# Optimization experiments

Measured on AMD Instinct MI355X. Metric: run time of the kernel, lower is better.

The kernel has to match this reference:

```python
import jax, jax.numpy as jnp
import numpy as np

N_NODES = 100000


def gcn_conv(x, W, b, src, dst, num_nodes):
    """PyG GCNConv: self-loops + symmetric norm + linear + scatter-add."""
    loop = jnp.arange(num_nodes, dtype=src.dtype)
    s = jnp.concatenate([src, loop])  # [E+N]
    d = jnp.concatenate([dst, loop])  # [E+N]
    # degree on destination column (edge_weight = 1)
    deg = jax.ops.segment_sum(jnp.ones_like(d, dtype=x.dtype), d,
                              num_segments=num_nodes)
    dinv = jnp.where(deg > 0, jax.lax.rsqrt(deg), 0.0)
    norm = dinv[s] * dinv[d]  # [E+N]
    h = x @ W  # [N, out] project before aggregation
    msg = h[s] * norm[:, None]  # gather + normalize
    out = jax.ops.segment_sum(msg, d, num_segments=num_nodes)  # scatter-add
    return out + b


def setup_inputs() -> dict:
    key = jax.random.key(0)
    k_x, k_e, k_w1, k_b1, k_w2, k_b2 = jax.random.split(key, 6)
    in_channels, hidden, out_dim = 128, 64, 2
    n_edges = 3200000
    x = jax.random.normal(k_x, (N_NODES, in_channels), dtype=jnp.float32)
    edge_index = jax.random.randint(k_e, (2, n_edges), 0, N_NODES, dtype=jnp.int64)
    # Glorot-style init for linear weights, zero bias (PyG default)
    W1 = jax.random.normal(k_w1, (in_channels, hidden), dtype=jnp.float32) * (1.0 / np.sqrt(in_channels))
    b1 = jnp.zeros((hidden,), dtype=jnp.float32)
    W2 = jax.random.normal(k_w2, (hidden, out_dim), dtype=jnp.float32) * (1.0 / np.sqrt(hidden))
    b2 = jnp.zeros((out_dim,), dtype=jnp.float32)
    return {"x": x, "edge_index": edge_index, "W1": W1, "b1": b1, "W2": W2, "b2": b2}


def reference(x, edge_index, W1, b1, W2, b2):
    src, dst = edge_index[0], edge_index[1]
    h = gcn_conv(x, W1, b1, src, dst, N_NODES)
    h = jax.nn.relu(h)
    # dropout(p=0.3) is identity in eval mode
    return gcn_conv(h, W2, b2, src, dst, N_NODES)
```

## Files before the change

kernel.cpp:

```cpp
#include <hip/hip_runtime.h>
#include <hip/hip_fp16.h>

#define IN_CH 128
#define HID 64
#define CHUNK1 16384
#define GBITS 8
#define SCAN_CHUNK 8192

__global__ __launch_bounds__(256) void k_p1count(const int* __restrict__ dst,
                                                 int* __restrict__ C,
                                                 int E, int G, int NB1) {
    __shared__ int lcnt[512];
    int t = threadIdx.x;
    for (int i = t; i < G; i += 256) lcnt[i] = 0;
    __syncthreads();
    int lo = blockIdx.x * CHUNK1;
    int hi = min(E, lo + CHUNK1);
    for (int e = lo + t; e < hi; e += 256) {
        int d = __builtin_nontemporal_load(dst + e);
        atomicAdd(&lcnt[d >> GBITS], 1);
    }
    __syncthreads();
    for (int g = t; g < G; g += 256) C[(size_t)g * NB1 + blockIdx.x] = lcnt[g];
}

__global__ __launch_bounds__(256) void k_scan_blocksum(const int* __restrict__ a,
                                                       int* __restrict__ bsum, int M) {
    int t = threadIdx.x;
    int base = blockIdx.x * SCAN_CHUNK + t * 32;
    int s = 0;
#pragma unroll
    for (int q = 0; q < 8; ++q) {
        int b = base + q * 4;
        if (b + 3 < M) {
            int4 v = *(const int4*)(a + b);
            s += v.x + v.y + v.z + v.w;
        } else {
            for (int i = 0; i < 4; ++i) if (b + i < M) s += a[b + i];
        }
    }
#pragma unroll
    for (int off = 32; off; off >>= 1) s += __shfl_down(s, off);
    __shared__ int ws[4];
    if ((t & 63) == 0) ws[t >> 6] = s;
    __syncthreads();
    if (t == 0) bsum[blockIdx.x] = ws[0] + ws[1] + ws[2] + ws[3];
}

__global__ __launch_bounds__(128) void k_scan_bsums(int* __restrict__ bsum, int nb) {
    __shared__ int sh[128];
    int t = threadIdx.x;
    int v = (t < nb) ? bsum[t] : 0;
    sh[t] = v;
    __syncthreads();
    for (int off = 1; off < 128; off <<= 1) {
        int u = (t >= off) ? sh[t - off] : 0;
        __syncthreads();
        sh[t] += u;
        __syncthreads();
    }
    if (t < nb) bsum[t] = (t == 0) ? 0 : sh[t - 1];
}

__global__ __launch_bounds__(256) void k_scan_apply(int* __restrict__ a,
                                                    const int* __restrict__ boff,
                                                    int M, int E) {
    int t = threadIdx.x;
    int base = blockIdx.x * SCAN_CHUNK + t * 32;
    int v[32];
    int tsum = 0;
#pragma unroll
    for (int q = 0; q < 8; ++q) {
        int b = base + q * 4;
        if (b + 3 < M) {
            int4 w = *(const int4*)(a + b);
            v[q * 4 + 0] = w.x; v[q * 4 + 1] = w.y; v[q * 4 + 2] = w.z; v[q * 4 + 3] = w.w;
        } else {
            for (int i = 0; i < 4; ++i) v[q * 4 + i] = (b + i < M) ? a[b + i] : 0;
        }
        tsum += v[q * 4] + v[q * 4 + 1] + v[q * 4 + 2] + v[q * 4 + 3];
    }
    __shared__ int sh[256];
    sh[t] = tsum;
    __syncthreads();
    for (int off = 1; off < 256; off <<= 1) {
        int u = (t >= off) ? sh[t - off] : 0;
        __syncthreads();
        sh[t] += u;
        __syncthreads();
    }
    int run = ((t == 0) ? 0 : sh[t - 1]) + boff[blockIdx.x];
#pragma unroll
    for (int q = 0; q < 8; ++q) {
        int b = base + q * 4;
        int o0 = run;            run += v[q * 4 + 0];
        int o1 = run;            run += v[q * 4 + 1];
        int o2 = run;            run += v[q * 4 + 2];
        int o3 = run;            run += v[q * 4 + 3];
        if (b + 3 < M) { *(int4*)(a + b) = make_int4(o0, o1, o2, o3); }
        else {
            if (b     < M) a[b]     = o0;
            if (b + 1 < M) a[b + 1] = o1;
            if (b + 2 < M) a[b + 2] = o2;
            if (b + 3 < M) a[b + 3] = o3;
        }
    }
    if (blockIdx.x == 0 && t == 0) a[M] = E;
}

__global__ __launch_bounds__(256) void k_p1scat(const int* __restrict__ src,
                                                const int* __restrict__ dst,
                                                const int* __restrict__ S,
                                                unsigned int* __restrict__ part,
                                                int E, int G, int NB1) {
    __shared__ int lcur[512];
    int t = threadIdx.x;
    for (int g = t; g < G; g += 256) lcur[g] = S[(size_t)g * NB1 + blockIdx.x];
    __syncthreads();
    int lo = blockIdx.x * CHUNK1;
    int hi = min(E, lo + CHUNK1);
    for (int e = lo + t; e < hi; e += 256) {
        int d = __builtin_nontemporal_load(dst + e);
        int s = __builtin_nontemporal_load(src + e);
        int pos = atomicAdd(&lcur[d >> GBITS], 1);
        part[pos] = ((unsigned)s << GBITS) | (unsigned)(d & ((1 << GBITS) - 1));
    }
}

__global__ __launch_bounds__(256) void k_p2(const unsigned int* __restrict__ part,
                                            const int* __restrict__ S,
                                            int* __restrict__ rowptr,
                                            float* __restrict__ dinv,
                                            int* __restrict__ esorted,
                                            int E, int N, int G, int NB1) {
    __shared__ int lcnt[256], lpre[256], lcur[256];
    int t = threadIdx.x;
    int g = blockIdx.x;
    int base = S[(size_t)g * NB1];
    int end  = (g == G - 1) ? E : S[(size_t)(g + 1) * NB1];
    lcnt[t] = 0;
    __syncthreads();
    for (int i = base + t; i < end; i += 256) {
        unsigned p = part[i];
        atomicAdd(&lcnt[p & 255], 1);
    }
    __syncthreads();
    int v = lcnt[t];
    lpre[t] = v;
    __syncthreads();
    for (int off = 1; off < 256; off <<= 1) {
        int u = (t >= off) ? lpre[t - off] : 0;
        __syncthreads();
        lpre[t] += u;
        __syncthreads();
    }
    int excl = (t == 0) ? 0 : lpre[t - 1];
    lcur[t] = base + excl;
    int node = (g << GBITS) + t;
    if (node < N) {
        rowptr[node] = base + excl;
        dinv[node] = rsqrtf(1.0f + (float)v);
    }
    if (g == 0 && t == 0) rowptr[N] = E;
    __syncthreads();
    for (int i = base + t; i < end; i += 256) {
        unsigned p = part[i];
        int pos = atomicAdd(&lcur[p & 255], 1);
        esorted[pos] = (int)(p >> GBITS);
    }
}

__global__ __launch_bounds__(256) void k_gemm1(const float* __restrict__ x,
                                               const float* __restrict__ W1,
                                               const float* __restrict__ dinv,
                                               __half* __restrict__ hp1h, int N) {
    __shared__ float sW[IN_CH * HID];
    __shared__ float sx[16 * IN_CH];
    const int tid = threadIdx.x;
    const int node0 = blockIdx.x * 16;

    {
        const float4* g = (const float4*)W1;
        float4* s = (float4*)sW;
        for (int i = tid; i < IN_CH * HID / 4; i += 256) s[i] = g[i];
    }
    {
        const float4* g = (const float4*)(x + (size_t)node0 * IN_CH);
        float4* s = (float4*)sx;
        for (int i = tid; i < 16 * IN_CH / 4; i += 256) s[i] = g[i];
    }
    __syncthreads();

    const int k  = tid & 63;
    const int n0 = tid >> 6;
    float a0 = 0.f, a1 = 0.f, a2 = 0.f, a3 = 0.f;
#pragma unroll 8
    for (int j = 0; j < IN_CH; ++j) {
        float w = sW[j * HID + k];
        a0 = fmaf(sx[(n0     ) * IN_CH + j], w, a0);
        a1 = fmaf(sx[(n0 +  4) * IN_CH + j], w, a1);
        a2 = fmaf(sx[(n0 +  8) * IN_CH + j], w, a2);
        a3 = fmaf(sx[(n0 + 12) * IN_CH + j], w, a3);
    }
    hp1h[(size_t)(node0 + n0     ) * HID + k] = __float2half(a0 * dinv[node0 + n0]);
    hp1h[(size_t)(node0 + n0 +  4) * HID + k] = __float2half(a1 * dinv[node0 + n0 + 4]);
    hp1h[(size_t)(node0 + n0 +  8) * HID + k] = __float2half(a2 * dinv[node0 + n0 + 8]);
    hp1h[(size_t)(node0 + n0 + 12) * HID + k] = __float2half(a3 * dinv[node0 + n0 + 12]);
}

__global__ __launch_bounds__(256) void k_agg1(const int* __restrict__ rowptr,
                                              const int* __restrict__ esorted,
                                              const __half2* __restrict__ hp1h,
                                              const float* __restrict__ dinv,
                                              const float* __restrict__ b1,
                                              const float* __restrict__ W2,
                                              float* __restrict__ hp2, int N) {
    int wid = (blockIdx.x * blockDim.x + threadIdx.x) >> 6;
    if (wid >= N) return;
    const int lane = threadIdx.x & 63;
    const int k32  = lane & 31;
    const int half = lane >> 5;
    int beg = rowptr[wid], end = rowptr[wid + 1];

    float a0x = 0.f, a0y = 0.f, a1x = 0.f, a1y = 0.f;
    float a2x = 0.f, a2y = 0.f, a3x = 0.f, a3y = 0.f;
    int e = beg;
    for (; e + 7 < end; e += 8) {
        int sa0 = esorted[e + 0], sb0 = esorted[e + 1];
        int sa1 = esorted[e + 2], sb1 = esorted[e + 3];
        int sa2 = esorted[e + 4], sb2 = esorted[e + 5];
        int sa3 = esorted[e + 6], sb3 = esorted[e + 7];
        int s0 = half ? sb0 : sa0;
        int s1 = half ? sb1 : sa1;
        int s2 = half ? sb2 : sa2;
        int s3 = half ? sb3 : sa3;
        float2 f0 = __half22float2(hp1h[(size_t)s0 * 32 + k32]);
        float2 f1 = __half22float2(hp1h[(size_t)s1 * 32 + k32]);
        float2 f2 = __half22float2(hp1h[(size_t)s2 * 32 + k32]);
        float2 f3 = __half22float2(hp1h[(size_t)s3 * 32 + k32]);
        a0x += f0.x; a0y += f0.y;
        a1x += f1.x; a1y += f1.y;
        a2x += f2.x; a2y += f2.y;
        a3x += f3.x; a3y += f3.y;
    }
    for (; e < end; e += 2) {
        int idx = e + half;
        int s = esorted[(idx < end) ? idx : e];
        float2 f = __half22float2(hp1h[(size_t)s * 32 + k32]);
        float w = (idx < end) ? 1.f : 0.f;
        a0x = fmaf(f.x, w, a0x);
        a0y = fmaf(f.y, w, a0y);
    }
    float ax = (a0x + a1x) + (a2x + a3x);
    float ay = (a0y + a1y) + (a2y + a3y);
    ax += __shfl_xor(ax, 32);
    ay += __shfl_xor(ay, 32);

    float2 fs = __half22float2(hp1h[(size_t)wid * 32 + k32]);
    ax += fs.x;
    ay += fs.y;

    float dj = dinv[wid];
    float2 bb = *(const float2*)(b1 + 2 * k32);
    float h0 = fmaxf(fmaf(dj, ax, bb.x), 0.0f);
    float h1 = fmaxf(fmaf(dj, ay, bb.y), 0.0f);
    float4 w4 = *(const float4*)(W2 + 4 * k32);
    float p0 = h0 * w4.x + h1 * w4.z;
    float p1 = h0 * w4.y + h1 * w4.w;
#pragma unroll
    for (int off = 32; off; off >>= 1) {
        p0 += __shfl_xor(p0, off);
        p1 += __shfl_xor(p1, off);
    }
    if (lane == 0) {
        hp2[(size_t)wid * 2 + 0] = p0 * 0.5f * dj;
        hp2[(size_t)wid * 2 + 1] = p1 * 0.5f * dj;
    }
}

__global__ __launch_bounds__(256) void k_agg2(const int* __restrict__ rowptr,
                                              const int* __restrict__ esorted,
                                              const float* __restrict__ hp2,
                                              const float* __restrict__ dinv,
                                              const float* __restrict__ b2,
                                              float* __restrict__ out, int N) {
    int gid = blockIdx.x * blockDim.x + threadIdx.x;
    int j = gid >> 3;
    if (j >= N) return;
    int l = gid & 7;
    int beg = rowptr[j], end = rowptr[j + 1];
    float ax = 0.f, ay = 0.f;
    for (int e = beg + l; e < end; e += 8) {
        int s = esorted[e];
        float2 v = *(const float2*)(hp2 + (size_t)s * 2);
        ax += v.x;
        ay += v.y;
    }
#pragma unroll
    for (int off = 1; off < 8; off <<= 1) {
        ax += __shfl_xor(ax, off);
        ay += __shfl_xor(ay, off);
    }
    if (l == 0) {
        float2 self = *(const float2*)(hp2 + (size_t)j * 2);
        float dj = dinv[j];
        out[(size_t)j * 2 + 0] = fmaf(dj, ax + self.x, b2[0]);
        out[(size_t)j * 2 + 1] = fmaf(dj, ay + self.y, b2[1]);
    }
}

extern "C" void kernel_launch(void* const* d_in, const int* in_sizes, int n_in,
                              void* d_out, int out_size, void* d_ws, size_t ws_size,
                              hipStream_t stream) {
    const float* x  = (const float*)d_in[0];
    const int*   ei = (const int*)d_in[1];
    const float* W1 = (const float*)d_in[2];
    const float* b1 = (const float*)d_in[3];
    const float* W2 = (const float*)d_in[4];
    const float* b2 = (const float*)d_in[5];
    float* out = (float*)d_out;

    const int N = in_sizes[0] / IN_CH;
    const int E = in_sizes[1] / 2;
    const int* src = ei;
    const int* dst = ei + E;

    const int G   = (N + 255) >> GBITS;
    const int NB1 = (E + CHUNK1 - 1) / CHUNK1;
    const int M   = G * NB1;
    const int NBs = (M + SCAN_CHUNK - 1) / SCAN_CHUNK;

    char* ws = (char*)d_ws;
    size_t o = 0;
    auto carve = [&](size_t bytes) -> char* {
        char* p = ws + o;
        o = (o + bytes + 255) & ~(size_t)255;
        return p;
    };
    int*          S       = (int*)carve(((size_t)M + 1) * 4);
    unsigned int* part    = (unsigned int*)carve((size_t)E * 4);
    int*          rowptr  = (int*)carve(((size_t)N + 1) * 4);
    float*        dinv    = (float*)carve((size_t)N * 4);
    int*          bsum    = (int*)carve(128 * 4);
    int*          esorted = (int*)carve((size_t)E * 4);
    __half*       hp1h    = (__half*)carve((size_t)N * HID * 2);
    float*        hp2     = (float*)carve((size_t)N * 2 * 4);
    (void)ws_size;

    k_p1count<<<NB1, 256, 0, stream>>>(dst, S, E, G, NB1);
    k_scan_blocksum<<<NBs, 256, 0, stream>>>(S, bsum, M);
    k_scan_bsums<<<1, 128, 0, stream>>>(bsum, NBs);
    k_scan_apply<<<NBs, 256, 0, stream>>>(S, bsum, M, E);
    k_p1scat<<<NB1, 256, 0, stream>>>(src, dst, S, part, E, G, NB1);
    k_p2<<<G, 256, 0, stream>>>(part, S, rowptr, dinv, esorted, E, N, G, NB1);

    k_gemm1<<<(N + 15) / 16, 256, 0, stream>>>(x, W1, dinv, hp1h, N);
    k_agg1<<<(unsigned)(((size_t)N * 64 + 255) / 256), 256, 0, stream>>>(
        rowptr, esorted, (const __half2*)hp1h, dinv, b1, W2, hp2, N);
    k_agg2<<<(unsigned)(((size_t)N * 8 + 255) / 256), 256, 0, stream>>>(
        rowptr, esorted, hp2, dinv, b2, out, N);
}
```

Measured before the change: 253.8 us.

## Double block size for sort kernels and sum neighbors in half2 in agg1

The partition, scatter and bucket-sort kernels now run with 512 threads per block instead of 256, with guards so the per-bucket scan still uses 256 threads. In k_agg1 each half-wave now handles 8 edges per iteration (16 per wave) and adds neighbor features pairwise in fp16 with __hadd2 before converting to fp32. Indexing also switches from 64-bit to 32-bit unsigned arithmetic. The fp16 partial sums reduce conversion and add work but lose accumulation precision, and the larger blocks change how many blocks fit per compute unit.

```diff
diff --git a/kernel.cpp b/kernel.cpp
--- a/kernel.cpp
+++ b/kernel.cpp
@@ -7,21 +7,21 @@
 #define GBITS 8
 #define SCAN_CHUNK 8192
 
-__global__ __launch_bounds__(256) void k_p1count(const int* __restrict__ dst,
+__global__ __launch_bounds__(512) void k_p1count(const int* __restrict__ dst,
                                                  int* __restrict__ C,
                                                  int E, int G, int NB1) {
     __shared__ int lcnt[512];
     int t = threadIdx.x;
-    for (int i = t; i < G; i += 256) lcnt[i] = 0;
+    for (int i = t; i < G; i += 512) lcnt[i] = 0;
     __syncthreads();
     int lo = blockIdx.x * CHUNK1;
     int hi = min(E, lo + CHUNK1);
-    for (int e = lo + t; e < hi; e += 256) {
+    for (int e = lo + t; e < hi; e += 512) {
         int d = __builtin_nontemporal_load(dst + e);
         atomicAdd(&lcnt[d >> GBITS], 1);
     }
     __syncthreads();
-    for (int g = t; g < G; g += 256) C[(size_t)g * NB1 + blockIdx.x] = lcnt[g];
+    for (int g = t; g < G; g += 512) C[(size_t)g * NB1 + blockIdx.x] = lcnt[g];
 }
 
 __global__ __launch_bounds__(256) void k_scan_blocksum(const int* __restrict__ a,
@@ -108,18 +108,18 @@
     if (blockIdx.x == 0 && t == 0) a[M] = E;
 }
 
-__global__ __launch_bounds__(256) void k_p1scat(const int* __restrict__ src,
+__global__ __launch_bounds__(512) void k_p1scat(const int* __restrict__ src,
                                                 const int* __restrict__ dst,
                                                 const int* __restrict__ S,
                                                 unsigned int* __restrict__ part,
                                                 int E, int G, int NB1) {
     __shared__ int lcur[512];
     int t = threadIdx.x;
-    for (int g = t; g < G; g += 256) lcur[g] = S[(size_t)g * NB1 + blockIdx.x];
+    for (int g = t; g < G; g += 512) lcur[g] = S[(size_t)g * NB1 + blockIdx.x];
     __syncthreads();
     int lo = blockIdx.x * CHUNK1;
     int hi = min(E, lo + CHUNK1);
-    for (int e = lo + t; e < hi; e += 256) {
+    for (int e = lo + t; e < hi; e += 512) {
         int d = __builtin_nontemporal_load(dst + e);
         int s = __builtin_nontemporal_load(src + e);
         int pos = atomicAdd(&lcur[d >> GBITS], 1);
@@ -127,7 +127,7 @@
     }
 }
 
-__global__ __launch_bounds__(256) void k_p2(const unsigned int* __restrict__ part,
+__global__ __launch_bounds__(512) void k_p2(const unsigned int* __restrict__ part,
                                             const int* __restrict__ S,
                                             int* __restrict__ rowptr,
                                             float* __restrict__ dinv,
@@ -138,32 +138,37 @@
     int g = blockIdx.x;
     int base = S[(size_t)g * NB1];
     int end  = (g == G - 1) ? E : S[(size_t)(g + 1) * NB1];
-    lcnt[t] = 0;
-    __syncthreads();
-    for (int i = base + t; i < end; i += 256) {
+    if (t < 256) lcnt[t] = 0;
+    __syncthreads();
+    for (int i = base + t; i < end; i += 512) {
         unsigned p = part[i];
         atomicAdd(&lcnt[p & 255], 1);
     }
     __syncthreads();
-    int v = lcnt[t];
-    lpre[t] = v;
+    int v = 0;
+    if (t < 256) {
+        v = lcnt[t];
+        lpre[t] = v;
+    }
     __syncthreads();
     for (int off = 1; off < 256; off <<= 1) {
-        int u = (t >= off) ? lpre[t - off] : 0;
-        __syncthreads();
-        lpre[t] += u;
-        __syncthreads();
-    }
-    int excl = (t == 0) ? 0 : lpre[t - 1];
-    lcur[t] = base + excl;
-    int node = (g << GBITS) + t;
-    if (node < N) {
-        rowptr[node] = base + excl;
-        dinv[node] = rsqrtf(1.0f + (float)v);
+        int u = (t >= off && t < 256) ? lpre[t - off] : 0;
+        __syncthreads();
+        if (t < 256) lpre[t] += u;
+        __syncthreads();
+    }
+    if (t < 256) {
+        int excl = (t == 0) ? 0 : lpre[t - 1];
+        lcur[t] = base + excl;
+        int node = (g << GBITS) + t;
+        if (node < N) {
+            rowptr[node] = base + excl;
+            dinv[node] = rsqrtf(1.0f + (float)v);
+        }
     }
     if (g == 0 && t == 0) rowptr[N] = E;
     __syncthreads();
-    for (int i = base + t; i < end; i += 256) {
+    for (int i = base + t; i < end; i += 512) {
         unsigned p = part[i];
         int pos = atomicAdd(&lcur[p & 255], 1);
         esorted[pos] = (int)(p >> GBITS);
@@ -222,41 +227,40 @@
     const int half = lane >> 5;
     int beg = rowptr[wid], end = rowptr[wid + 1];
 
-    float a0x = 0.f, a0y = 0.f, a1x = 0.f, a1y = 0.f;
-    float a2x = 0.f, a2y = 0.f, a3x = 0.f, a3y = 0.f;
+    float ax = 0.f, ay = 0.f;
     int e = beg;
-    for (; e + 7 < end; e += 8) {
-        int sa0 = esorted[e + 0], sb0 = esorted[e + 1];
-        int sa1 = esorted[e + 2], sb1 = esorted[e + 3];
-        int sa2 = esorted[e + 4], sb2 = esorted[e + 5];
-        int sa3 = esorted[e + 6], sb3 = esorted[e + 7];
-        int s0 = half ? sb0 : sa0;
-        int s1 = half ? sb1 : sa1;
-        int s2 = half ? sb2 : sa2;
-        int s3 = half ? sb3 : sa3;
-        float2 f0 = __half22float2(hp1h[(size_t)s0 * 32 + k32]);
-        float2 f1 = __half22float2(hp1h[(size_t)s1 * 32 + k32]);
-        float2 f2 = __half22float2(hp1h[(size_t)s2 * 32 + k32]);
-        float2 f3 = __half22float2(hp1h[(size_t)s3 * 32 + k32]);
-        a0x += f0.x; a0y += f0.y;
-        a1x += f1.x; a1y += f1.y;
-        a2x += f2.x; a2y += f2.y;
-        a3x += f3.x; a3y += f3.y;
-    }
-    for (; e < end; e += 2) {
-        int idx = e + half;
-        int s = esorted[(idx < end) ? idx : e];
-        float2 f = __half22float2(hp1h[(size_t)s * 32 + k32]);
-        float w = (idx < end) ? 1.f : 0.f;
-        a0x = fmaf(f.x, w, a0x);
-        a0y = fmaf(f.y, w, a0y);
-    }
-    float ax = (a0x + a1x) + (a2x + a3x);
-    float ay = (a0y + a1y) + (a2y + a3y);
+    for (; e + 15 < end; e += 16) {
+        const int* ep = esorted + e + 8 * half;
+        int s0 = ep[0], s1 = ep[1], s2 = ep[2], s3 = ep[3];
+        int s4 = ep[4], s5 = ep[5], s6 = ep[6], s7 = ep[7];
+        __half2 h0 = hp1h[(unsigned)(s0 * 32 + k32)];
+        __half2 h1 = hp1h[(unsigned)(s1 * 32 + k32)];
+        __half2 h2 = hp1h[(unsigned)(s2 * 32 + k32)];
+        __half2 h3 = hp1h[(unsigned)(s3 * 32 + k32)];
+        h0 = __hadd2(h0, hp1h[(unsigned)(s4 * 32 + k32)]);
+        h1 = __hadd2(h1, hp1h[(unsigned)(s5 * 32 + k32)]);
+        h2 = __hadd2(h2, hp1h[(unsigned)(s6 * 32 + k32)]);
+        h3 = __hadd2(h3, hp1h[(unsigned)(s7 * 32 + k32)]);
+        float2 f0 = __half22float2(__hadd2(h0, h1));
+        float2 f1 = __half22float2(__hadd2(h2, h3));
+        ax += f0.x + f1.x;
+        ay += f0.y + f1.y;
+    }
+    for (; e + 1 < end; e += 2) {
+        int s = esorted[e + half];
+        float2 f = __half22float2(hp1h[(unsigned)(s * 32 + k32)]);
+        ax += f.x;
+        ay += f.y;
+    }
+    if (e < end) {
+        int s = esorted[e];
+        float2 f = __half22float2(hp1h[(unsigned)(s * 32 + k32)]);
+        if (half == 0) { ax += f.x; ay += f.y; }
+    }
     ax += __shfl_xor(ax, 32);
     ay += __shfl_xor(ay, 32);
 
-    float2 fs = __half22float2(hp1h[(size_t)wid * 32 + k32]);
+    float2 fs = __half22float2(hp1h[(unsigned)(wid * 32 + k32)]);
     ax += fs.x;
     ay += fs.y;
 
@@ -347,12 +351,12 @@
     float*        hp2     = (float*)carve((size_t)N * 2 * 4);
     (void)ws_size;
 
-    k_p1count<<<NB1, 256, 0, stream>>>(dst, S, E, G, NB1);
+    k_p1count<<<NB1, 512, 0, stream>>>(dst, S, E, G, NB1);
     k_scan_blocksum<<<NBs, 256, 0, stream>>>(S, bsum, M);
     k_scan_bsums<<<1, 128, 0, stream>>>(bsum, NBs);
     k_scan_apply<<<NBs, 256, 0, stream>>>(S, bsum, M, E);
-    k_p1scat<<<NB1, 256, 0, stream>>>(src, dst, S, part, E, G, NB1);
-    k_p2<<<G, 256, 0, stream>>>(part, S, rowptr, dinv, esorted, E, N, G, NB1);
+    k_p1scat<<<NB1, 512, 0, stream>>>(src, dst, S, part, E, G, NB1);
+    k_p2<<<G, 512, 0, stream>>>(part, S, rowptr, dinv, esorted, E, N, G, NB1);
 
     k_gemm1<<<(N + 15) / 16, 256, 0, stream>>>(x, W1, dinv, hp1h, N);
     k_agg1<<<(unsigned)(((size_t)N * 64 + 255) / 256), 256, 0, stream>>>(
```

Result: faster. 233.1 us (-8.2%).
